# Kernel tuning notes

Hardware: AMD Instinct MI355X
Metric: run time of the kernel (lower is better)

Reference implementation:

```python
import jax, jax.numpy as jnp
import numpy as np

MARGIN = 0.8  # TripletMarginMiner(margin=0.8, type_of_triplets='semihard')
Z_DIM = 512
N_CONCEPT = 64
NUM_TASK, NUM_SHOT, NUM_WAY = 16, 5, 5


def _triplet_indices(num_shot, num_way):
    # labels = torch.arange(num_way).repeat(num_shot) -> tile pattern
    labels = np.tile(np.arange(num_way), num_shot)
    N = labels.shape[0]
    same = labels[:, None] == labels[None, :]
    pos = same & ~np.eye(N, dtype=bool)          # a != p, same label
    neg = ~same                                  # different label
    a, p, n = np.nonzero(pos[:, :, None] & neg[:, None, :])  # all candidate triplets
    return jnp.asarray(a), jnp.asarray(p), jnp.asarray(n)


def setup_inputs() -> dict:
    key = jax.random.key(0)
    ks = jax.random.split(key, 12)
    d = Z_DIM
    s = lambda fan: 1.0 / np.sqrt(fan)
    inp = {
        'input_data': jax.random.normal(ks[0], (NUM_TASK, NUM_SHOT, NUM_WAY, d), jnp.float32),
        # proj_inner: Linear(3d -> 2d), ReLU, Linear(2d -> d)
        'W1': jax.random.normal(ks[1], (3 * d, 2 * d), jnp.float32) * s(3 * d),
        'b1': jnp.zeros((2 * d,), jnp.float32),
        'W2': jax.random.normal(ks[2], (2 * d, d), jnp.float32) * s(2 * d),
        'b2': jnp.zeros((d,), jnp.float32),
        # proj_outer: Linear(d -> 2d), ReLU, Linear(2d -> d)
        'W3': jax.random.normal(ks[3], (d, 2 * d), jnp.float32) * s(d),
        'b3': jnp.zeros((2 * d,), jnp.float32),
        'W4': jax.random.normal(ks[4], (2 * d, d), jnp.float32) * s(2 * d),
        'b4': jnp.zeros((d,), jnp.float32),
        # cls: Linear(d -> n_concept)
        'Wc': jax.random.normal(ks[5], (d, N_CONCEPT), jnp.float32) * s(d),
        'bc': jnp.zeros((N_CONCEPT,), jnp.float32),
    }
    return inp


def reference(input_data, W1, b1, W2, b2, W3, b3, W4, b4, Wc, bc):
    num_task, num_shot, num_way, d = input_data.shape
    x = input_data.reshape(num_task, num_shot * num_way, d)  # [K, N, d]
    a, p, n = _triplet_indices(num_shot, num_way)            # fixed triplet set [T]

    # --- semihard mining (no grad; binary mask so no grad path anyway) ---
    # LpDistance default: normalize embeddings, then L2 distance
    xn = x / jnp.linalg.norm(x, axis=-1, keepdims=True)
    sq = jnp.sum(xn * xn, axis=-1)                           # [K, N]
    D2 = sq[:, :, None] + sq[:, None, :] - 2.0 * jnp.einsum('kid,kjd->kij', xn, xn)
    D = jnp.sqrt(jnp.clip(D2, 0.0))                          # [K, N, N]
    tm = D[:, a, n] - D[:, a, p]                             # an_dist - ap_dist, [K, T]
    mask = ((tm > 0.0) & (tm <= MARGIN)).astype(x.dtype)     # semihard: 0 < margin <= 0.8

    # --- gather triplet embeddings (unnormalized), concat [x_a, x_p, x_n] ---
    feat = jnp.concatenate([x[:, a], x[:, p], x[:, n]], axis=-1)  # [K, T, 3d]

    # proj_inner then masked sum over mined triplets per task
    h = jax.nn.relu(feat @ W1 + b1) @ W2 + b2                # [K, T, d]
    pooled = jnp.einsum('ktd,kt->kd', h, mask)               # [K, d]

    o = jax.nn.relu(pooled @ W3 + b3) @ W4 + b4              # [K, d]
    score = o @ Wc + bc                                      # [K, n_concept]
    return jax.nn.softmax(score, axis=-1)
```

## Files before the change

kernel.cpp:

```cpp
#include <hip/hip_runtime.h>
#include <math.h>

#define NT 16
#define NR 25
#define DZ 512
#define D2Z 1024
#define NC 64

typedef short bf16x8 __attribute__((ext_vector_type(8)));
typedef float f32x4  __attribute__((ext_vector_type(4)));

#define TP  76
#define XSP 520
#define CP  68

static __device__ inline unsigned short f2bf(float v) {
    union { float f; unsigned u; } x; x.f = v;
    unsigned r = x.u + 0x7fffu + ((x.u >> 16) & 1u);
    return (unsigned short)(r >> 16);
}
static __device__ inline float bf2f(unsigned short h) {
    union { float f; unsigned u; } x; x.u = ((unsigned)h) << 16; return x.f;
}

__global__ __launch_bounds__(256) void k_prep(
    const float* __restrict__ x, const float* __restrict__ W1,
    unsigned short* __restrict__ W1h, unsigned short* __restrict__ W1l,
    float* __restrict__ Dm)
{
    __shared__ unsigned short th[64 * TP], tl[64 * TP];
    int vb = blockIdx.x;
    int tid = threadIdx.x;

    if (vb < 384) {
        int r0 = (vb % 24) * 64;
        int j0 = (vb / 24) * 64;
        int c  = r0 >> 9;
        int rb = r0 & 511;

        #pragma unroll
        for (int it = 0; it < 4; it++) {
            int rl = (tid >> 4) + it * 16;
            int jj = (tid & 15) * 4;
            float4 v = *(const float4*)(W1 + (size_t)(r0 + rl) * D2Z + j0 + jj);
            unsigned short h0 = f2bf(v.x), h1 = f2bf(v.y), h2 = f2bf(v.z), h3 = f2bf(v.w);
            th[rl * TP + jj + 0] = h0; tl[rl * TP + jj + 0] = f2bf(v.x - bf2f(h0));
            th[rl * TP + jj + 1] = h1; tl[rl * TP + jj + 1] = f2bf(v.y - bf2f(h1));
            th[rl * TP + jj + 2] = h2; tl[rl * TP + jj + 2] = f2bf(v.z - bf2f(h2));
            th[rl * TP + jj + 3] = h3; tl[rl * TP + jj + 3] = f2bf(v.w - bf2f(h3));
        }
        __syncthreads();

        #pragma unroll
        for (int it = 0; it < 4; it++) {
            int jl = (tid >> 4) + it * 16;
            int r4 = (tid & 15) * 4;
            ushort4 hv = make_ushort4(th[(r4+0)*TP + jl], th[(r4+1)*TP + jl],
                                      th[(r4+2)*TP + jl], th[(r4+3)*TP + jl]);
            ushort4 lv = make_ushort4(tl[(r4+0)*TP + jl], tl[(r4+1)*TP + jl],
                                      tl[(r4+2)*TP + jl], tl[(r4+3)*TP + jl]);
            size_t dst = ((size_t)c * D2Z + j0 + jl) * DZ + rb + r4;
            *(ushort4*)(W1h + dst) = hv;
            *(ushort4*)(W1l + dst) = lv;
        }
    } else {
        int i = vb - 384;
        int k = i & 15, a = i >> 4;
        int lane = tid & 63;
        int w    = tid >> 6;
        const float* xk = x + (size_t)k * NR * DZ;

        const float4* xap = (const float4*)(xk + a * DZ);
        float4 a0 = xap[lane];
        float4 a1 = xap[lane + 64];

        float sa = a0.x*a0.x + a0.y*a0.y + a0.z*a0.z + a0.w*a0.w
                 + a1.x*a1.x + a1.y*a1.y + a1.z*a1.z + a1.w*a1.w;
        #pragma unroll
        for (int off = 32; off; off >>= 1) sa += __shfl_xor(sa, off);
        float inva = 1.0f / sqrtf(sa);
        a0.x *= inva; a0.y *= inva; a0.z *= inva; a0.w *= inva;
        a1.x *= inva; a1.y *= inva; a1.z *= inva; a1.w *= inva;
        float sqa = a0.x*a0.x + a0.y*a0.y + a0.z*a0.z + a0.w*a0.w
                  + a1.x*a1.x + a1.y*a1.y + a1.z*a1.z + a1.w*a1.w;
        #pragma unroll
        for (int off = 32; off; off >>= 1) sqa += __shfl_xor(sqa, off);

        for (int j = w; j < NR; j += 4) {
            const float4* xjp = (const float4*)(xk + j * DZ);
            float4 j0 = xjp[lane];
            float4 j1 = xjp[lane + 64];
            float sj = j0.x*j0.x + j0.y*j0.y + j0.z*j0.z + j0.w*j0.w
                     + j1.x*j1.x + j1.y*j1.y + j1.z*j1.z + j1.w*j1.w;
            #pragma unroll
            for (int off = 32; off; off >>= 1) sj += __shfl_xor(sj, off);
            float invj = 1.0f / sqrtf(sj);
            j0.x *= invj; j0.y *= invj; j0.z *= invj; j0.w *= invj;
            j1.x *= invj; j1.y *= invj; j1.z *= invj; j1.w *= invj;

            float sqj = j0.x*j0.x + j0.y*j0.y + j0.z*j0.z + j0.w*j0.w
                      + j1.x*j1.x + j1.y*j1.y + j1.z*j1.z + j1.w*j1.w;
            float dij = a0.x*j0.x + a0.y*j0.y + a0.z*j0.z + a0.w*j0.w
                      + a1.x*j1.x + a1.y*j1.y + a1.z*j1.z + a1.w*j1.w;
            #pragma unroll
            for (int off = 32; off; off >>= 1) {
                sqj += __shfl_xor(sqj, off);
                dij += __shfl_xor(dij, off);
            }
            float d2 = sqa + sqj - 2.0f * dij;
            float d  = sqrtf(fmaxf(d2, 0.0f));
            if (lane == 0) Dm[((size_t)k * NR + a) * NR + j] = d;
        }
    }
}

__global__ __launch_bounds__(256, 2) void k_fused(
    const float* __restrict__ x,
    const unsigned short* __restrict__ W1h, const unsigned short* __restrict__ W1l,
    const float* __restrict__ b1, const float* __restrict__ Dm,
    float* __restrict__ G)
{
    __shared__ unsigned short xs_h[25 * XSP], xs_l[25 * XSP];
    __shared__ float Ct[75 * CP];
    __shared__ float Dm_s[NR * NR];
    __shared__ float red[4][64];

    int bid = blockIdx.x;
    int k  = bid >> 4;
    int jt = bid & 15;
    int j0 = jt * 64;

    int tid  = threadIdx.x;
    int lane = tid & 63;
    int w    = tid >> 6;
    int q    = lane >> 4;
    int ln16 = lane & 15;

    for (int idx = tid; idx < NR * NR; idx += 256)
        Dm_s[idx] = Dm[(size_t)k * NR * NR + idx];

    for (int g = tid; g < NR * 64; g += 256) {
        int row = g >> 6;
        int c8  = (g & 63) * 8;
        const float* xp = x + ((size_t)k * NR + row) * DZ + c8;
        float4 v0 = *(const float4*)(xp);
        float4 v1 = *(const float4*)(xp + 4);
        unsigned short h;
        ushort4 ha, hb, la, lb;
        h = f2bf(v0.x); ha.x = h; la.x = f2bf(v0.x - bf2f(h));
        h = f2bf(v0.y); ha.y = h; la.y = f2bf(v0.y - bf2f(h));
        h = f2bf(v0.z); ha.z = h; la.z = f2bf(v0.z - bf2f(h));
        h = f2bf(v0.w); ha.w = h; la.w = f2bf(v0.w - bf2f(h));
        h = f2bf(v1.x); hb.x = h; lb.x = f2bf(v1.x - bf2f(h));
        h = f2bf(v1.y); hb.y = h; lb.y = f2bf(v1.y - bf2f(h));
        h = f2bf(v1.z); hb.z = h; lb.z = f2bf(v1.z - bf2f(h));
        h = f2bf(v1.w); hb.w = h; lb.w = f2bf(v1.w - bf2f(h));
        *(ushort4*)&xs_h[row * XSP + c8]     = ha;
        *(ushort4*)&xs_h[row * XSP + c8 + 4] = hb;
        *(ushort4*)&xs_l[row * XSP + c8]     = la;
        *(ushort4*)&xs_l[row * XSP + c8 + 4] = lb;
    }
    __syncthreads();

    int rowA1 = 16 + ln16;
    if (rowA1 > 24) rowA1 = 24;

    const unsigned short* wb_h = W1h + ((size_t)j0 + w * 16 + ln16) * DZ + q * 8;
    const unsigned short* wb_l = W1l + ((size_t)j0 + w * 16 + ln16) * DZ + q * 8;

    for (int c = 0; c < 3; c++) {
        f32x4 acc0 = (f32x4){0.f,0.f,0.f,0.f};
        f32x4 acc1 = (f32x4){0.f,0.f,0.f,0.f};
        const unsigned short* wch = wb_h + (size_t)c * D2Z * DZ;
        const unsigned short* wcl = wb_l + (size_t)c * D2Z * DZ;

        #pragma unroll
        for (int kc = 0; kc < 16; kc++) {
            int kog = kc * 32 + q * 8;
            bf16x8 b_h = *(const bf16x8*)(wch + kc * 32);
            bf16x8 b_l = *(const bf16x8*)(wcl + kc * 32);
            bf16x8 a0h = *(const bf16x8*)&xs_h[ln16 * XSP + kog];
            bf16x8 a0l = *(const bf16x8*)&xs_l[ln16 * XSP + kog];
            bf16x8 a1h = *(const bf16x8*)&xs_h[rowA1 * XSP + kog];
            bf16x8 a1l = *(const bf16x8*)&xs_l[rowA1 * XSP + kog];
            acc0 = __builtin_amdgcn_mfma_f32_16x16x32_bf16(a0h, b_h, acc0, 0, 0, 0);
            acc0 = __builtin_amdgcn_mfma_f32_16x16x32_bf16(a0h, b_l, acc0, 0, 0, 0);
            acc0 = __builtin_amdgcn_mfma_f32_16x16x32_bf16(a0l, b_h, acc0, 0, 0, 0);
            acc1 = __builtin_amdgcn_mfma_f32_16x16x32_bf16(a1h, b_h, acc1, 0, 0, 0);
            acc1 = __builtin_amdgcn_mfma_f32_16x16x32_bf16(a1h, b_l, acc1, 0, 0, 0);
            acc1 = __builtin_amdgcn_mfma_f32_16x16x32_bf16(a1l, b_h, acc1, 0, 0, 0);
        }

        int col = w * 16 + ln16;
        #pragma unroll
        for (int r = 0; r < 4; r++) {
            int r0 = q * 4 + r;
            Ct[(c * 25 + r0) * CP + col] = acc0[r];
            int r1 = 16 + q * 4 + r;
            if (r1 < 25) Ct[(c * 25 + r1) * CP + col] = acc1[r];
        }
    }
    __syncthreads();

    int j = tid & 63;
    int h = tid >> 6;
    float b1v = b1[j0 + j];

    float a2v[NR], a3v[NR];
    #pragma unroll
    for (int i = 0; i < NR; i++) a2v[i] = Ct[(25 + i) * CP + j];
    #pragma unroll
    for (int i = 0; i < NR; i++) a3v[i] = Ct[(50 + i) * CP + j];

    float acc = 0.0f;
    #pragma unroll
    for (int a = 0; a < NR; a++) {
        const int qa = a % 5, mdiv = a / 5;
        int m = h + (h >= mdiv);
        int p = qa + 5 * m;
        float a1  = Ct[a * CP + j];
        float dap = Dm_s[a * NR + p];
        float s = a1 + a2v[p] + b1v;
        #pragma unroll
        for (int ng = 0; ng < 5; ng++) {
            #pragma unroll
            for (int o = 0; o < 4; o++) {
                int n = ng * 5 + o + (o >= qa);
                float tm = Dm_s[a * NR + n] - dap;
                bool sel = (tm > 0.0f) && (tm <= 0.8f);
                float pre = fmaxf(s + a3v[n], 0.0f);
                float msk = sel ? 1.0f : 0.0f;
                acc = fmaf(msk, pre, acc);
            }
        }
    }
    red[h][j] = acc;
    __syncthreads();
    if (tid < 64)
        G[(size_t)k * D2Z + j0 + tid] = red[0][tid] + red[1][tid]
                                      + red[2][tid] + red[3][tid];
}

__global__ __launch_bounds__(256) void k_pooled(const float* __restrict__ G,
                                                const float* __restrict__ Dm,
                                                const float* __restrict__ W2,
                                                const float* __restrict__ b2,
                                                float* __restrict__ pooled)
{
    int bx = blockIdx.x, k = blockIdx.y;
    int tid = threadIdx.x, lane = tid & 63, kc = tid >> 6;
    int col = bx * 64 + lane;

    const float* Dk = Dm + (size_t)k * NR * NR;
    float cntv = 0.0f;
    for (int idx = tid; idx < 2000; idx += 256) {
        int a   = idx / 80;
        int rem = idx - a * 80;
        int mi  = rem / 20;
        int nn  = rem - mi * 20;
        int qa = a % 5, mdiv = a / 5;
        int m = mi + (mi >= mdiv);
        int p = qa + 5 * m;
        int ng = nn >> 2, o = nn & 3;
        int n = ng * 5 + o + (o >= qa);
        float tm = Dk[a * NR + n] - Dk[a * NR + p];
        cntv += ((tm > 0.0f) && (tm <= 0.8f)) ? 1.0f : 0.0f;
    }
    #pragma unroll
    for (int off = 32; off; off >>= 1) cntv += __shfl_xor(cntv, off);

    __shared__ float red[4][64];
    __shared__ float cred[4];
    if (lane == 0) cred[kc] = cntv;

    const float* Gk = G + (size_t)k * D2Z;
    float a0 = 0.f, a1 = 0.f, a2 = 0.f, a3 = 0.f;
    int j0 = kc * 256;
    #pragma unroll 4
    for (int jj = j0; jj < j0 + 256; jj += 4) {
        a0 = fmaf(Gk[jj+0], W2[(size_t)(jj+0) * DZ + col], a0);
        a1 = fmaf(Gk[jj+1], W2[(size_t)(jj+1) * DZ + col], a1);
        a2 = fmaf(Gk[jj+2], W2[(size_t)(jj+2) * DZ + col], a2);
        a3 = fmaf(Gk[jj+3], W2[(size_t)(jj+3) * DZ + col], a3);
    }
    red[kc][lane] = (a0 + a1) + (a2 + a3);
    __syncthreads();
    if (tid < 64) {
        float cnt = cred[0] + cred[1] + cred[2] + cred[3];
        float s = red[0][lane] + red[1][lane] + red[2][lane] + red[3][lane];
        s += cnt * b2[col];
        pooled[(size_t)k * DZ + col] = s;
    }
}

__global__ __launch_bounds__(256) void k_u(const float* __restrict__ pooled,
                                           const float* __restrict__ W3,
                                           const float* __restrict__ b3,
                                           float* __restrict__ u)
{
    int bx = blockIdx.x, k = blockIdx.y;
    int tid = threadIdx.x, lane = tid & 63, kc = tid >> 6;
    int col = bx * 64 + lane;

    const float* Pk = pooled + (size_t)k * DZ;
    float a0 = 0.f, a1 = 0.f, a2 = 0.f, a3 = 0.f;
    int s0 = kc * 128;
    #pragma unroll 4
    for (int s = s0; s < s0 + 128; s += 4) {
        a0 = fmaf(Pk[s+0], W3[(size_t)(s+0) * D2Z + col], a0);
        a1 = fmaf(Pk[s+1], W3[(size_t)(s+1) * D2Z + col], a1);
        a2 = fmaf(Pk[s+2], W3[(size_t)(s+2) * D2Z + col], a2);
        a3 = fmaf(Pk[s+3], W3[(size_t)(s+3) * D2Z + col], a3);
    }
    __shared__ float red[4][64];
    red[kc][lane] = (a0 + a1) + (a2 + a3);
    __syncthreads();
    if (tid < 64) {
        float v = red[0][lane] + red[1][lane] + red[2][lane] + red[3][lane] + b3[col];
        u[(size_t)k * D2Z + col] = fmaxf(v, 0.0f);
    }
}

__global__ __launch_bounds__(256) void k_o(const float* __restrict__ u,
                                           const float* __restrict__ W4,
                                           const float* __restrict__ b4,
                                           float* __restrict__ o)
{
    int bx = blockIdx.x, k = blockIdx.y;
    int tid = threadIdx.x, lane = tid & 63, kc = tid >> 6;
    int col = bx * 64 + lane;

    const float* Uk = u + (size_t)k * D2Z;
    float a0 = 0.f, a1 = 0.f, a2 = 0.f, a3 = 0.f;
    int j0 = kc * 256;
    #pragma unroll 4
    for (int jj = j0; jj < j0 + 256; jj += 4) {
        a0 = fmaf(Uk[jj+0], W4[(size_t)(jj+0) * DZ + col], a0);
        a1 = fmaf(Uk[jj+1], W4[(size_t)(jj+1) * DZ + col], a1);
        a2 = fmaf(Uk[jj+2], W4[(size_t)(jj+2) * DZ + col], a2);
        a3 = fmaf(Uk[jj+3], W4[(size_t)(jj+3) * DZ + col], a3);
    }
    __shared__ float red[4][64];
    red[kc][lane] = (a0 + a1) + (a2 + a3);
    __syncthreads();
    if (tid < 64) {
        o[(size_t)k * DZ + col] = red[0][lane] + red[1][lane] + red[2][lane]
                                + red[3][lane] + b4[col];
    }
}

__global__ __launch_bounds__(256) void k_score(const float* __restrict__ o,
                                               const float* __restrict__ Wc,
                                               const float* __restrict__ bc,
                                               float* __restrict__ out)
{
    int k = blockIdx.x;
    int tid = threadIdx.x, oc = tid & 63, kc = tid >> 6;

    const float* Ok = o + (size_t)k * DZ;
    float a0 = 0.f, a1 = 0.f, a2 = 0.f, a3 = 0.f;
    int r0 = kc * 128;
    #pragma unroll 4
    for (int rr = r0; rr < r0 + 128; rr += 4) {
        a0 = fmaf(Ok[rr+0], Wc[(size_t)(rr+0) * NC + oc], a0);
        a1 = fmaf(Ok[rr+1], Wc[(size_t)(rr+1) * NC + oc], a1);
        a2 = fmaf(Ok[rr+2], Wc[(size_t)(rr+2) * NC + oc], a2);
        a3 = fmaf(Ok[rr+3], Wc[(size_t)(rr+3) * NC + oc], a3);
    }
    __shared__ float red[4][64];
    red[kc][oc] = (a0 + a1) + (a2 + a3);
    __syncthreads();
    if (tid < 64) {
        float sc = bc[tid] + red[0][tid] + red[1][tid] + red[2][tid] + red[3][tid];
        float m = sc;
        #pragma unroll
        for (int off = 32; off; off >>= 1) m = fmaxf(m, __shfl_xor(m, off));
        float e = expf(sc - m);
        float ss = e;
        #pragma unroll
        for (int off = 32; off; off >>= 1) ss += __shfl_xor(ss, off);
        out[k * NC + tid] = e / ss;
    }
}

extern "C" void kernel_launch(void* const* d_in, const int* in_sizes, int n_in,
                              void* d_out, int out_size, void* d_ws, size_t ws_size,
                              hipStream_t stream)
{
    const float* x  = (const float*)d_in[0];
    const float* W1 = (const float*)d_in[1];
    const float* b1 = (const float*)d_in[2];
    const float* W2 = (const float*)d_in[3];
    const float* b2 = (const float*)d_in[4];
    const float* W3 = (const float*)d_in[5];
    const float* b3 = (const float*)d_in[6];
    const float* W4 = (const float*)d_in[7];
    const float* b4 = (const float*)d_in[8];
    const float* Wc = (const float*)d_in[9];
    const float* bc = (const float*)d_in[10];
    float* out = (float*)d_out;

    float* ws     = (float*)d_ws;
    float* Dm     = ws;
    float* G      = ws + 10016;
    float* pooled = ws + 26400;
    float* uu     = pooled + 8192;
    float* oo     = uu + 16384;
    unsigned short* W1h = (unsigned short*)(oo + 8192);
    unsigned short* W1l = W1h + 3 * D2Z * DZ;

    k_prep  <<<784,            256, 0, stream>>>(x, W1, W1h, W1l, Dm);
    k_fused <<<256,            256, 0, stream>>>(x, W1h, W1l, b1, Dm, G);
    k_pooled<<<dim3(8, NT),    256, 0, stream>>>(G, Dm, W2, b2, pooled);
    k_u     <<<dim3(16, NT),   256, 0, stream>>>(pooled, W3, b3, uu);
    k_o     <<<dim3(8, NT),    256, 0, stream>>>(uu, W4, b4, oo);
    k_score <<<NT,             256, 0, stream>>>(oo, Wc, bc, out);
}
```

Baseline: 151.7 us.

## Split k_fused GEMM across K halves and halve column tile to double grid

The fused triplet kernel now covers 32 output columns per block instead of 64, so the grid grows from 256 to 512 blocks. Each block's four waves are arranged as 2 column groups by 2 K-halves, and the two partial products are summed from shared memory. The masked triplet accumulation is redistributed over 8 thread slices that stride over anchors. The aim is more parallelism and better CU occupancy on a small-grid kernel, at the cost of loading and converting x twice as often and an extra shared-memory reduction.

```diff
diff --git a/kernel.cpp b/kernel.cpp
--- a/kernel.cpp
+++ b/kernel.cpp
@@ -12,7 +12,7 @@
 
 #define TP  76
 #define XSP 520
-#define CP  68
+#define CP2 36
 
 static __device__ inline unsigned short f2bf(float v) {
     union { float f; unsigned u; } x; x.f = v;
@@ -121,18 +121,20 @@
     float* __restrict__ G)
 {
     __shared__ unsigned short xs_h[25 * XSP], xs_l[25 * XSP];
-    __shared__ float Ct[75 * CP];
+    __shared__ float Ct[2][75 * CP2];
     __shared__ float Dm_s[NR * NR];
-    __shared__ float red[4][64];
+    __shared__ float red[8][32];
 
     int bid = blockIdx.x;
-    int k  = bid >> 4;
-    int jt = bid & 15;
-    int j0 = jt * 64;
+    int k  = bid >> 5;
+    int jt = bid & 31;
+    int j0 = jt * 32;
 
     int tid  = threadIdx.x;
     int lane = tid & 63;
     int w    = tid >> 6;
+    int wn   = w & 1;
+    int wk   = w >> 1;
     int q    = lane >> 4;
     int ln16 = lane & 15;
 
@@ -165,8 +167,8 @@
     int rowA1 = 16 + ln16;
     if (rowA1 > 24) rowA1 = 24;
 
-    const unsigned short* wb_h = W1h + ((size_t)j0 + w * 16 + ln16) * DZ + q * 8;
-    const unsigned short* wb_l = W1l + ((size_t)j0 + w * 16 + ln16) * DZ + q * 8;
+    const unsigned short* wb_h = W1h + ((size_t)j0 + wn * 16 + ln16) * DZ + wk * 256 + q * 8;
+    const unsigned short* wb_l = W1l + ((size_t)j0 + wn * 16 + ln16) * DZ + wk * 256 + q * 8;
 
     for (int c = 0; c < 3; c++) {
         f32x4 acc0 = (f32x4){0.f,0.f,0.f,0.f};
@@ -175,8 +177,8 @@
         const unsigned short* wcl = wb_l + (size_t)c * D2Z * DZ;
 
         #pragma unroll
-        for (int kc = 0; kc < 16; kc++) {
-            int kog = kc * 32 + q * 8;
+        for (int kc = 0; kc < 8; kc++) {
+            int kog = wk * 256 + kc * 32 + q * 8;
             bf16x8 b_h = *(const bf16x8*)(wch + kc * 32);
             bf16x8 b_l = *(const bf16x8*)(wcl + kc * 32);
             bf16x8 a0h = *(const bf16x8*)&xs_h[ln16 * XSP + kog];
@@ -191,36 +193,39 @@
             acc1 = __builtin_amdgcn_mfma_f32_16x16x32_bf16(a1l, b_h, acc1, 0, 0, 0);
         }
 
-        int col = w * 16 + ln16;
+        int col = wn * 16 + ln16;
         #pragma unroll
         for (int r = 0; r < 4; r++) {
             int r0 = q * 4 + r;
-            Ct[(c * 25 + r0) * CP + col] = acc0[r];
+            Ct[wk][(c * 25 + r0) * CP2 + col] = acc0[r];
             int r1 = 16 + q * 4 + r;
-            if (r1 < 25) Ct[(c * 25 + r1) * CP + col] = acc1[r];
-        }
-    }
-    __syncthreads();
-
-    int j = tid & 63;
-    int h = tid >> 6;
+            if (r1 < 25) Ct[wk][(c * 25 + r1) * CP2 + col] = acc1[r];
+        }
+    }
+    __syncthreads();
+
+    int j  = tid & 31;
+    int s  = tid >> 5;
+    int mi = s & 3;
+    int ap = s >> 2;
     float b1v = b1[j0 + j];
 
     float a2v[NR], a3v[NR];
     #pragma unroll
-    for (int i = 0; i < NR; i++) a2v[i] = Ct[(25 + i) * CP + j];
+    for (int i = 0; i < NR; i++)
+        a2v[i] = Ct[0][(25 + i) * CP2 + j] + Ct[1][(25 + i) * CP2 + j];
     #pragma unroll
-    for (int i = 0; i < NR; i++) a3v[i] = Ct[(50 + i) * CP + j];
+    for (int i = 0; i < NR; i++)
+        a3v[i] = Ct[0][(50 + i) * CP2 + j] + Ct[1][(50 + i) * CP2 + j];
 
     float acc = 0.0f;
-    #pragma unroll
-    for (int a = 0; a < NR; a++) {
+    for (int a = ap; a < NR; a += 2) {
         const int qa = a % 5, mdiv = a / 5;
-        int m = h + (h >= mdiv);
+        int m = mi + (mi >= mdiv);
         int p = qa + 5 * m;
-        float a1  = Ct[a * CP + j];
+        float a1  = Ct[0][a * CP2 + j] + Ct[1][a * CP2 + j];
         float dap = Dm_s[a * NR + p];
-        float s = a1 + a2v[p] + b1v;
+        float sv = a1 + a2v[p] + b1v;
         #pragma unroll
         for (int ng = 0; ng < 5; ng++) {
             #pragma unroll
@@ -228,17 +233,20 @@
                 int n = ng * 5 + o + (o >= qa);
                 float tm = Dm_s[a * NR + n] - dap;
                 bool sel = (tm > 0.0f) && (tm <= 0.8f);
-                float pre = fmaxf(s + a3v[n], 0.0f);
+                float pre = fmaxf(sv + a3v[n], 0.0f);
                 float msk = sel ? 1.0f : 0.0f;
                 acc = fmaf(msk, pre, acc);
             }
         }
     }
-    red[h][j] = acc;
-    __syncthreads();
-    if (tid < 64)
-        G[(size_t)k * D2Z + j0 + tid] = red[0][tid] + red[1][tid]
-                                      + red[2][tid] + red[3][tid];
+    red[s][j] = acc;
+    __syncthreads();
+    if (tid < 32) {
+        float g = 0.0f;
+        #pragma unroll
+        for (int t = 0; t < 8; t++) g += red[t][tid];
+        G[(size_t)k * D2Z + j0 + tid] = g;
+    }
 }
 
 __global__ __launch_bounds__(256) void k_pooled(const float* __restrict__ G,
@@ -410,7 +418,7 @@
     unsigned short* W1l = W1h + 3 * D2Z * DZ;
 
     k_prep  <<<784,            256, 0, stream>>>(x, W1, W1h, W1l, Dm);
-    k_fused <<<256,            256, 0, stream>>>(x, W1h, W1l, b1, Dm, G);
+    k_fused <<<512,            256, 0, stream>>>(x, W1h, W1l, b1, Dm, G);
     k_pooled<<<dim3(8, NT),    256, 0, stream>>>(G, Dm, W2, b2, pooled);
     k_u     <<<dim3(16, NT),   256, 0, stream>>>(pooled, W3, b3, uu);
     k_o     <<<dim3(8, NT),    256, 0, stream>>>(uu, W4, b4, oo);
```

New measurement: 185.7 us. 1.22x slower.
